# Kernel tuning notes

Measured on AMD Instinct MI355X. Metric: run time of the kernel, lower is better.

Reference implementation:

```python
import jax, jax.numpy as jnp
import numpy as np

C = 256
G = 32  # GroupNorm groups
EPS = 1e-6


def setup_inputs() -> dict:
    key = jax.random.key(0)
    ks = jax.random.split(key, 11)
    B, H, W = 4, 64, 64
    scale = 0.02
    return {
        "x": jax.random.normal(ks[0], (B, C, H, W), dtype=jnp.float32),
        "gn_scale": jnp.ones((C,), jnp.float32),
        "gn_bias": jnp.zeros((C,), jnp.float32),
        "wq": jax.random.normal(ks[1], (C, C), jnp.float32) * scale,
        "bq": jnp.zeros((C,), jnp.float32),
        "wk": jax.random.normal(ks[2], (C, C), jnp.float32) * scale,
        "bk": jnp.zeros((C,), jnp.float32),
        "wv": jax.random.normal(ks[3], (C, C), jnp.float32) * scale,
        "bv": jnp.zeros((C,), jnp.float32),
        "wp": jax.random.normal(ks[4], (C, C), jnp.float32) * scale,
        "bp": jnp.zeros((C,), jnp.float32),
    }


def _group_norm(x, scale, bias):
    b, c, h, w = x.shape
    xr = x.reshape(b, G, c // G, h, w)
    mu = jnp.mean(xr, axis=(2, 3, 4), keepdims=True)
    var = jnp.var(xr, axis=(2, 3, 4), keepdims=True)
    xn = ((xr - mu) * jax.lax.rsqrt(var + EPS)).reshape(b, c, h, w)
    return xn * scale[None, :, None, None] + bias[None, :, None, None]


def _conv1x1(x, w, bch):
    # 1x1 conv == channel-mixing matmul; w is (out_ch, in_ch)
    return jnp.einsum('bchw,dc->bdhw', x, w) + bch[None, :, None, None]


def reference(x, gn_scale, gn_bias, wq, bq, wk, bk, wv, bv, wp, bp):
    b, c, h, w = x.shape
    hn = _group_norm(x, gn_scale, gn_bias)
    q = _conv1x1(hn, wq, bq).reshape(b, c, h * w)  # (b,c,N)
    k = _conv1x1(hn, wk, bk).reshape(b, c, h * w)
    v = _conv1x1(hn, wv, bv).reshape(b, c, h * w)
    # attn[b,i,j] = softmax_j( q_i . k_j / sqrt(c) )
    attn = jax.nn.softmax(jnp.einsum('bci,bcj->bij', q, k) * (c ** -0.5), axis=-1)
    A = jnp.einsum('bcj,bij->bci', v, attn).reshape(b, c, h, w)
    return x + _conv1x1(A, wp, bp)
```

## Files before the change

kernel.cpp:

```cpp
#include <hip/hip_runtime.h>
#include <stdint.h>

#define Bn 4
#define Cn 256
#define Gn 32
#define Nn 4096
#define CGn 8

typedef unsigned short u16;
typedef __attribute__((ext_vector_type(8))) short short8;
typedef __attribute__((ext_vector_type(4))) short short4v;
typedef __attribute__((ext_vector_type(4))) float f32x4;
typedef __attribute__((ext_vector_type(16))) float f32x16;

__device__ __forceinline__ u16 f2bf(float x) {
  uint32_t u = __float_as_uint(x);
  u += 0x7fffu + ((u >> 16) & 1u);
  return (u16)(u >> 16);
}
__device__ __forceinline__ float b2f(u16 v) {
  return __uint_as_float(((uint32_t)v) << 16);
}

__device__ __forceinline__ void gl_lds16(const void* g, void* l) {
  __builtin_amdgcn_global_load_lds(
      (__attribute__((address_space(1))) void*)(uintptr_t)g,
      (__attribute__((address_space(3))) void*)(uintptr_t)l, 16, 0, 0);
}

__device__ __forceinline__ int sw512(int row, int cb) { return row * 512 + ((cb ^ (row & 7)) * 16); }

__global__ void k_cs(const float* __restrict__ wq, const float* __restrict__ wk,
                     const float* __restrict__ wv, const float* __restrict__ wp,
                     const float* __restrict__ bq, const float* __restrict__ bk,
                     const float* __restrict__ bv, const float* __restrict__ x,
                     u16* __restrict__ wqkv, u16* __restrict__ wpb,
                     float* __restrict__ bqkv, float* __restrict__ stats) {
  if (blockIdx.x < 256) {
    const float s = 0.09016844005556021f;
    int i = blockIdx.x * 256 + threadIdx.x;
    wqkv[i]          = f2bf(wq[i] * s);
    wqkv[i + 65536]  = f2bf(wk[i]);
    wqkv[i + 131072] = f2bf(wv[i]);
    wpb[i]           = f2bf(wp[i]);
    if (i < 256) { bqkv[i] = bq[i] * s; bqkv[i + 256] = bk[i]; bqkv[i + 512] = bv[i]; }
  } else {
    int blk = blockIdx.x - 256;
    int grp = blk >> 2, part = blk & 3;
    const float4* base = (const float4*)(x + (size_t)grp * (CGn * Nn) + part * 8192);
    float s = 0.f, s2 = 0.f;
    for (int i = threadIdx.x; i < 2048; i += 256) {
      float4 v = base[i];
      s  += v.x + v.y + v.z + v.w;
      s2 += v.x * v.x + v.y * v.y + v.z * v.z + v.w * v.w;
    }
#pragma unroll
    for (int m = 1; m < 64; m <<= 1) { s += __shfl_xor(s, m, 64); s2 += __shfl_xor(s2, m, 64); }
    __shared__ float ps[4], ps2[4];
    int w = threadIdx.x >> 6;
    if ((threadIdx.x & 63) == 0) { ps[w] = s; ps2[w] = s2; }
    __syncthreads();
    if (threadIdx.x == 0) {
      stats[grp * 8 + part * 2]     = ps[0] + ps[1] + ps[2] + ps[3];
      stats[grp * 8 + part * 2 + 1] = ps2[0] + ps2[1] + ps2[2] + ps2[3];
    }
  }
}

__global__ void k_apply(const float* __restrict__ x, const float* __restrict__ stats,
                        const float* __restrict__ gsc, const float* __restrict__ gbi,
                        u16* __restrict__ hnT) {
  __shared__ __align__(16) char smem[32768];
  __shared__ float smu[Gn], srs[Gn];
  int n0 = blockIdx.x * 64;
  int b = blockIdx.y;
  int tid = threadIdx.x;
  if (tid < Gn) {
    float S = 0.f, S2 = 0.f;
#pragma unroll
    for (int p = 0; p < 4; ++p) {
      S  += stats[(b * Gn + tid) * 8 + p * 2];
      S2 += stats[(b * Gn + tid) * 8 + p * 2 + 1];
    }
    const float inv = 1.f / (CGn * Nn);
    float mu = S * inv;
    float var = S2 * inv - mu * mu;
    smu[tid] = mu;
    srs[tid] = rsqrtf(var + 1e-6f);
  }
  __syncthreads();
  int nl = (tid & 15) * 4;
  int cbase = tid >> 4;
  for (int pass = 0; pass < 16; ++pass) {
    int c = pass * 16 + cbase;
    float4 v = *(const float4*)(x + (size_t)b * Cn * Nn + (size_t)c * Nn + n0 + nl);
    int g = c >> 3;
    float sc = gsc[c] * srs[g];
    float bi = gbi[c] - smu[g] * sc;
    float vals[4] = {v.x, v.y, v.z, v.w};
#pragma unroll
    for (int i = 0; i < 4; ++i) {
      int row = nl + i;
      int off = row * 512 + ((((c >> 3) + row) & 31) * 16) + (c & 7) * 2;
      *(u16*)(smem + off) = f2bf(vals[i] * sc + bi);
    }
  }
  __syncthreads();
#pragma unroll
  for (int p = 0; p < 8; ++p) {
    int idx = p * 256 + tid;
    int row = idx >> 5, pc = idx & 31;
    int gc = (pc - row) & 31;
    short8 v8 = *(const short8*)(smem + row * 512 + pc * 16);
    *(short8*)(hnT + ((size_t)b * Nn + n0 + row) * Cn + gc * 8) = v8;
  }
}

__global__ __launch_bounds__(256, 2)
void k_qkv(const u16* __restrict__ wqkv, const float* __restrict__ bqkv,
           const u16* __restrict__ hnT, u16* __restrict__ qT, u16* __restrict__ kT,
           u16* __restrict__ vv) {
  __shared__ __align__(16) char smem[65536];
  const int tid = threadIdx.x, lane = tid & 63, w = tid >> 6;
  const int quad = (lane >> 4) & 3, low = lane & 15;
  const int d0 = blockIdx.y * 64, b = blockIdx.z;
  const int n_base = blockIdx.x * 256;
  const int which = d0 >> 8;
  const int dl0 = d0 & 255;
  const u16* hb = hnT + (size_t)b * Nn * Cn;
  const int scol = lane & 31;

#define QKV_STAGE(bsel, nt)                                                     \
  {                                                                             \
    _Pragma("unroll") for (int s = 0; s < 8; ++s) {                             \
      int r = w * 16 + s * 2 + (lane >> 5);                                     \
      int gc = (scol - r) & 31;                                                 \
      gl_lds16(hb + (size_t)(n_base + (nt) * 64 + r) * Cn + gc * 8,             \
               smem + (bsel) * 32768 + (w * 16 + s * 2) * 512);                 \
    }                                                                           \
  }

  QKV_STAGE(0, 0);
  short8 af[8];
  {
    const u16* wrow = wqkv + (size_t)(d0 + w * 16 + low) * Cn + quad * 8;
#pragma unroll
    for (int kk = 0; kk < 8; ++kk) af[kk] = *(const short8*)(wrow + kk * 32);
  }
  float bias[4];
#pragma unroll
  for (int r = 0; r < 4; ++r) bias[r] = bqkv[d0 + w * 16 + quad * 4 + r];

  for (int nt = 0; nt < 4; ++nt) {
    if (nt < 3) {
      QKV_STAGE((nt + 1) & 1, nt + 1);
      asm volatile("s_waitcnt vmcnt(10)" ::: "memory");
    } else {
      asm volatile("s_waitcnt vmcnt(0)" ::: "memory");
    }
    asm volatile("s_barrier" ::: "memory");
    char* buf = smem + (nt & 1) * 32768;
    f32x4 acc[4] = {{0.f,0.f,0.f,0.f},{0.f,0.f,0.f,0.f},{0.f,0.f,0.f,0.f},{0.f,0.f,0.f,0.f}};
#pragma unroll
    for (int kk = 0; kk < 8; ++kk)
#pragma unroll
      for (int t = 0; t < 4; ++t) {
        int row = t * 16 + low;
        short8 bf = *(const short8*)(buf + row * 512 + (((kk * 4 + quad) + row) & 31) * 16);
        acc[t] = __builtin_amdgcn_mfma_f32_16x16x32_bf16(af[kk], bf, acc[t], 0, 0, 0);
      }
    asm volatile("s_barrier" ::: "memory");
    char* Q = buf + w * 8192;
    if (which == 2) {
#pragma unroll
      for (int t = 0; t < 4; ++t)
#pragma unroll
        for (int rp = 0; rp < 2; ++rp) {
          uint32_t wv2;
          float f0 = acc[t][2 * rp] + bias[2 * rp];
          float f1 = acc[t][2 * rp + 1] + bias[2 * rp + 1];
          asm("v_cvt_pk_bf16_f32 %0, %1, %2" : "=v"(wv2) : "v"(f0), "v"(f1));
          *(u16*)(Q + (quad * 4 + 2 * rp) * 144 + t * 32 + low * 2) = (u16)wv2;
          *(u16*)(Q + (quad * 4 + 2 * rp + 1) * 144 + t * 32 + low * 2) = (u16)(wv2 >> 16);
        }
#pragma unroll
      for (int s = 0; s < 2; ++s) {
        int slot = s * 64 + lane;
        int row = slot >> 3, ch = slot & 7;
        short8 v8 = *(const short8*)(Q + row * 144 + ch * 16);
        *(short8*)(vv + (size_t)b * Cn * Nn + (size_t)(dl0 + w * 16 + row) * Nn +
                   n_base + nt * 64 + ch * 8) = v8;
      }
    } else {
#pragma unroll
      for (int t = 0; t < 4; ++t) {
        union { uint32_t u[2]; short4v s; } pk;
        float f0 = acc[t][0] + bias[0], f1 = acc[t][1] + bias[1];
        float f2 = acc[t][2] + bias[2], f3 = acc[t][3] + bias[3];
        asm("v_cvt_pk_bf16_f32 %0, %1, %2" : "=v"(pk.u[0]) : "v"(f0), "v"(f1));
        asm("v_cvt_pk_bf16_f32 %0, %1, %2" : "=v"(pk.u[1]) : "v"(f2), "v"(f3));
        *(short4v*)(Q + (t * 16 + low) * 48 + quad * 8) = pk.s;
      }
      u16* dst = (which == 0 ? qT : kT) + (size_t)b * Nn * Cn;
#pragma unroll
      for (int s = 0; s < 2; ++s) {
        int slot = s * 64 + lane;
        int row = slot >> 1, half = slot & 1;
        short8 v8 = *(const short8*)(Q + row * 48 + half * 16);
        *(short8*)(dst + (size_t)(n_base + nt * 64 + row) * Cn + dl0 + w * 16 + half * 8) = v8;
      }
    }
  }
#undef QKV_STAGE
}

__device__ __forceinline__ void flash_stage(char* smem, int bsel, const u16* kTb,
                                            const u16* vb, int j0, int w, int lo,
                                            int kr, int vr, int vp) {
  char* ksb = smem + bsel * 32768;
  char* vsb = ksb + 16384;
#pragma unroll
  for (int s = 0; s < 4; ++s) {
    int j = kr + s * 2;
    int gc = (lo - j) & 31;
    gl_lds16(kTb + (size_t)(j0 + j) * Cn + gc * 8, ksb + (w * 8 + s * 2) * 512);
  }
#pragma unroll
  for (int s = 0; s < 4; ++s) {
    int c = vr + s * 16;
    int gc = (vp - c - (c >> 2)) & 3;
    gl_lds16(vb + (size_t)c * Nn + j0 + gc * 8, vsb + (w * 64 + s * 16) * 64);
  }
}

__global__ __launch_bounds__(256, 2)
void k_flash(const u16* __restrict__ qT, const u16* __restrict__ kT,
             const u16* __restrict__ vv, u16* __restrict__ Op0,
             u16* __restrict__ Op1, u16* __restrict__ Op2, u16* __restrict__ Op3,
             float* __restrict__ lrow) {
  __shared__ __align__(16) char smem[65536];
  const int tid = threadIdx.x, lane = tid & 63, w = tid >> 6;
  const int lo = lane & 31, hi = lane >> 5;
  const int i0 = blockIdx.x * 128;
  const int b = blockIdx.y, jh = blockIdx.z;
  const u16* qTb = qT + (size_t)b * Nn * Cn;
  const u16* kTb = kT + (size_t)b * Nn * Cn;
  const u16* vb  = vv + (size_t)b * Cn * Nn;
  const int u7 = lo + hi;
  const int u9 = lo + hi + (lo >> 2);
  const int kr = w * 8 + hi;
  const int vr = w * 64 + (lane >> 2);
  const int vp = lane & 3;

  flash_stage(smem, 0, kTb, vb, jh * 1024, w, lo, kr, vr, vp);

  short8 qf[16];
  {
    const u16* qrow = qTb + (size_t)(i0 + w * 32 + lo) * Cn + hi * 8;
#pragma unroll
    for (int ks = 0; ks < 16; ++ks) qf[ks] = *(const short8*)(qrow + ks * 16);
  }
  f32x16 Oa[8];
#pragma unroll
  for (int ct = 0; ct < 8; ++ct)
#pragma unroll
    for (int e = 0; e < 16; ++e) Oa[ct][e] = 0.f;
  float l_ = 0.f;

  for (int jt = 0; jt < 32; ++jt) {
    if (jt < 31) {
      flash_stage(smem, (jt + 1) & 1, kTb, vb, jh * 1024 + (jt + 1) * 32, w, lo, kr, vr, vp);
      asm volatile("s_waitcnt vmcnt(8)" ::: "memory");
    } else {
      asm volatile("s_waitcnt vmcnt(0)" ::: "memory");
    }
    asm volatile("s_barrier" ::: "memory");
    const char* ksb = smem + (jt & 1) * 32768;
    const char* vsb = ksb + 16384;

    f32x16 S0;
#pragma unroll
    for (int e = 0; e < 16; ++e) S0[e] = 0.f;
    __builtin_amdgcn_s_setprio(1);
#pragma unroll
    for (int ks = 0; ks < 16; ++ks) {
      int ch = (ks * 2 + u7) & 31;
      short8 a0 = *(const short8*)(ksb + lo * 512 + ch * 16);
      S0 = __builtin_amdgcn_mfma_f32_32x32x16_bf16(a0, qf[ks], S0, 0, 0, 0);
    }
    __builtin_amdgcn_s_setprio(0);
    uint32_t Pp[8];
#pragma unroll
    for (int g = 0; g < 8; ++g) {
      float p0 = __builtin_amdgcn_exp2f(S0[2 * g]);
      float p1 = __builtin_amdgcn_exp2f(S0[2 * g + 1]);
      l_ += p0 + p1;
      asm("v_cvt_pk_bf16_f32 %0, %1, %2" : "=v"(Pp[g]) : "v"(p0), "v"(p1));
    }
#pragma unroll
    for (int kst = 0; kst < 2; ++kst) {
      uint32_t x0 = Pp[4 * kst], x1 = Pp[4 * kst + 1];
      uint32_t y0 = Pp[4 * kst + 2], y1 = Pp[4 * kst + 3];
      asm("v_permlane32_swap_b32 %0, %1" : "+v"(x0), "+v"(y0));
      asm("v_permlane32_swap_b32 %0, %1" : "+v"(x1), "+v"(y1));
      union { uint32_t u[4]; short8 s8; } pu;
      pu.u[0] = x0;
      pu.u[1] = x1;
      pu.u[2] = y0;
      pu.u[3] = y1;
      int ch = (kst * 2 + u9) & 3;
      __builtin_amdgcn_s_setprio(1);
#pragma unroll
      for (int ct = 0; ct < 8; ++ct) {
        short8 vf = *(const short8*)(vsb + (ct * 32 + lo) * 64 + ch * 16);
        Oa[ct] = __builtin_amdgcn_mfma_f32_32x32x16_bf16(vf, pu.s8, Oa[ct], 0, 0, 0);
      }
      __builtin_amdgcn_s_setprio(0);
    }
    asm volatile("s_barrier" ::: "memory");
  }

  l_ += __shfl_xor(l_, 32, 64);
  if (hi == 0)
    lrow[(size_t)jh * (Bn * Nn) + (size_t)b * Nn + i0 + w * 32 + lo] = l_;
  float invl = __builtin_amdgcn_rcpf(l_);
  __syncthreads();
#pragma unroll
  for (int ct = 0; ct < 8; ++ct)
#pragma unroll
    for (int g = 0; g < 4; ++g) {
      union { uint32_t u[2]; short4v s; } pk;
      float f0 = Oa[ct][g * 4 + 0] * invl, f1 = Oa[ct][g * 4 + 1] * invl;
      float f2 = Oa[ct][g * 4 + 2] * invl, f3 = Oa[ct][g * 4 + 3] * invl;
      asm("v_cvt_pk_bf16_f32 %0, %1, %2" : "=v"(pk.u[0]) : "v"(f0), "v"(f1));
      asm("v_cvt_pk_bf16_f32 %0, %1, %2" : "=v"(pk.u[1]) : "v"(f2), "v"(f3));
      int chv = (ct * 4 + g + lo) & 31;
      *(short4v*)(smem + w * 16384 + lo * 512 + chv * 16 + hi * 8) = pk.s;
    }
  __syncthreads();
  u16* Opj = (jh == 0) ? Op0 : (jh == 1) ? Op1 : (jh == 2) ? Op2 : Op3;
  u16* Ob = Opj + ((size_t)b * Nn + i0 + w * 32) * (size_t)Cn;
#pragma unroll
  for (int s = 0; s < 16; ++s) {
    int rr = s * 2 + hi;
    short8 v8 = *(const short8*)(smem + w * 16384 + rr * 512 + lo * 16);
    int gc = (lo - rr) & 31;
    *(short8*)(Ob + (size_t)rr * Cn + gc * 8) = v8;
  }
}

__global__ __launch_bounds__(256, 2)
void k_proj(const u16* __restrict__ wpb, const float* __restrict__ bp,
            const u16* __restrict__ O0, const u16* __restrict__ O1,
            const u16* __restrict__ O2, const u16* __restrict__ O3,
            const float* __restrict__ lrow,
            const float* __restrict__ x, float* __restrict__ out) {
  __shared__ __align__(16) char smem[16384];
  int tid = threadIdx.x, lane = tid & 63, w = tid >> 6, quad = lane >> 4, low = lane & 15;
  int n0 = blockIdx.x * 32, b = blockIdx.z;
#pragma unroll
  for (int p = 0; p < 4; ++p) {
    int slot = p * 256 + tid;
    int row = slot >> 5, pc = slot & 31;
    int gcb = pc ^ (row & 7);
    size_t gbase = ((size_t)b * Nn + n0 + row) * Cn + gcb * 8;
    short8 a0 = *(const short8*)(O0 + gbase);
    short8 a1 = *(const short8*)(O1 + gbase);
    short8 a2 = *(const short8*)(O2 + gbase);
    short8 a3 = *(const short8*)(O3 + gbase);
    int rrow = b * Nn + n0 + row;
    float L = lrow[rrow] + lrow[Bn * Nn + rrow] + lrow[2 * Bn * Nn + rrow] +
              lrow[3 * Bn * Nn + rrow];
    float inv = __builtin_amdgcn_rcpf(L);
    short8 o;
#pragma unroll
    for (int i = 0; i < 8; ++i)
      o[i] = (short)f2bf((b2f((u16)a0[i]) + b2f((u16)a1[i]) + b2f((u16)a2[i]) +
                          b2f((u16)a3[i])) * inv);
    *(short8*)(smem + row * 512 + pc * 16) = o;
  }
  __syncthreads();
  for (int dg = 0; dg < 4; ++dg) {
    short8 af[8];
    {
      const u16* wrow = wpb + (size_t)(dg * 64 + w * 16 + low) * Cn + quad * 8;
#pragma unroll
      for (int kk = 0; kk < 8; ++kk) af[kk] = *(const short8*)(wrow + kk * 32);
    }
    f32x4 acc[2] = {{0.f,0.f,0.f,0.f},{0.f,0.f,0.f,0.f}};
#pragma unroll
    for (int kk = 0; kk < 8; ++kk)
#pragma unroll
      for (int t = 0; t < 2; ++t) {
        short8 bf = *(const short8*)(smem + sw512(t * 16 + low, kk * 4 + quad));
        acc[t] = __builtin_amdgcn_mfma_f32_16x16x32_bf16(af[kk], bf, acc[t], 0, 0, 0);
      }
    int dloc = dg * 64 + w * 16 + quad * 4;
#pragma unroll
    for (int t = 0; t < 2; ++t)
#pragma unroll
      for (int r = 0; r < 4; ++r) {
        size_t idx = (size_t)b * Cn * Nn + (size_t)(dloc + r) * Nn + n0 + t * 16 + low;
        out[idx] = x[idx] + acc[t][r] + bp[dloc + r];
      }
  }
}

extern "C" void kernel_launch(void* const* d_in, const int* in_sizes, int n_in,
                              void* d_out, int out_size, void* d_ws, size_t ws_size,
                              hipStream_t stream) {
  const float* x   = (const float*)d_in[0];
  const float* gsc = (const float*)d_in[1];
  const float* gbi = (const float*)d_in[2];
  const float* wq  = (const float*)d_in[3];
  const float* bq  = (const float*)d_in[4];
  const float* wk  = (const float*)d_in[5];
  const float* bk  = (const float*)d_in[6];
  const float* wv  = (const float*)d_in[7];
  const float* bv  = (const float*)d_in[8];
  const float* wp  = (const float*)d_in[9];
  const float* bp  = (const float*)d_in[10];
  float* out = (float*)d_out;

  char* ws = (char*)d_ws;
  u16*   wqkv  = (u16*)(ws + 0);
  u16*   wpb   = (u16*)(ws + 393216);
  float* bqkv  = (float*)(ws + 524288);
  float* stats = (float*)(ws + 527360);
  float* lrow  = (float*)(ws + 532480);
  u16*   hnT   = (u16*)(ws + 1048576);
  u16*   qT    = (u16*)(ws + 9437184);
  u16*   kT    = (u16*)(ws + 17825792);
  u16*   vv    = (u16*)(ws + 26214400);
  u16*   Op1   = (u16*)(ws + 34603008);
  u16*   Op2   = (u16*)(ws + 42991616);
  u16*   Op3   = (u16*)(ws + 51380224);

  k_cs<<<768, 256, 0, stream>>>(wq, wk, wv, wp, bq, bk, bv, x, wqkv, wpb, bqkv, stats);
  k_apply<<<dim3(64, 4), 256, 0, stream>>>(x, stats, gsc, gbi, hnT);
  k_qkv<<<dim3(16, 12, 4), 256, 0, stream>>>(wqkv, bqkv, hnT, qT, kT, vv);
  k_flash<<<dim3(32, 4, 4), 256, 0, stream>>>(qT, kT, vv, hnT , Op1, Op2, Op3, lrow);
  k_proj<<<dim3(128, 1, 4), 256, 0, stream>>>(wpb, bp, hnT , Op1, Op2, Op3, lrow, x, out);
}
```

Measured before the change: 193.1 us.

## Restructure QKV projection so each block loads a 32-row hn tile once and loops over all output channels

The QKV kernel used to split output channels across the grid, so every block re-staged a 256-row hn tile with double buffering. Now each block stages one 32-row hn tile into LDS once and loops over all 12 groups of 64 output channels, streaming the weights from global or cache. LDS use drops and launch bounds rise to 4 blocks per CU for more occupancy. The cost is that weight fragments are reloaded for every channel group and the weight-load latency is not pipelined. The LDS staging slots are reused between groups without a barrier, but they are private to each wave.

After: 205.7 us. 6.5% more time.

```diff
diff --git a/kernel.cpp b/kernel.cpp
--- a/kernel.cpp
+++ b/kernel.cpp
@@ -116,84 +116,68 @@
   }
 }
 
-__global__ __launch_bounds__(256, 2)
+__global__ __launch_bounds__(256, 4)
 void k_qkv(const u16* __restrict__ wqkv, const float* __restrict__ bqkv,
            const u16* __restrict__ hnT, u16* __restrict__ qT, u16* __restrict__ kT,
            u16* __restrict__ vv) {
-  __shared__ __align__(16) char smem[65536];
+  __shared__ __align__(16) char smem[24576];
   const int tid = threadIdx.x, lane = tid & 63, w = tid >> 6;
   const int quad = (lane >> 4) & 3, low = lane & 15;
-  const int d0 = blockIdx.y * 64, b = blockIdx.z;
-  const int n_base = blockIdx.x * 256;
-  const int which = d0 >> 8;
-  const int dl0 = d0 & 255;
+  const int n0 = blockIdx.x * 32, b = blockIdx.y;
   const u16* hb = hnT + (size_t)b * Nn * Cn;
-  const int scol = lane & 31;
-
-#define QKV_STAGE(bsel, nt)                                                     \
-  {                                                                             \
-    _Pragma("unroll") for (int s = 0; s < 8; ++s) {                             \
-      int r = w * 16 + s * 2 + (lane >> 5);                                     \
-      int gc = (scol - r) & 31;                                                 \
-      gl_lds16(hb + (size_t)(n_base + (nt) * 64 + r) * Cn + gc * 8,             \
-               smem + (bsel) * 32768 + (w * 16 + s * 2) * 512);                 \
-    }                                                                           \
-  }
-
-  QKV_STAGE(0, 0);
-  short8 af[8];
   {
-    const u16* wrow = wqkv + (size_t)(d0 + w * 16 + low) * Cn + quad * 8;
-#pragma unroll
-    for (int kk = 0; kk < 8; ++kk) af[kk] = *(const short8*)(wrow + kk * 32);
-  }
-  float bias[4];
-#pragma unroll
-  for (int r = 0; r < 4; ++r) bias[r] = bqkv[d0 + w * 16 + quad * 4 + r];
-
-  for (int nt = 0; nt < 4; ++nt) {
-    if (nt < 3) {
-      QKV_STAGE((nt + 1) & 1, nt + 1);
-      asm volatile("s_waitcnt vmcnt(10)" ::: "memory");
-    } else {
-      asm volatile("s_waitcnt vmcnt(0)" ::: "memory");
-    }
-    asm volatile("s_barrier" ::: "memory");
-    char* buf = smem + (nt & 1) * 32768;
-    f32x4 acc[4] = {{0.f,0.f,0.f,0.f},{0.f,0.f,0.f,0.f},{0.f,0.f,0.f,0.f},{0.f,0.f,0.f,0.f}};
+    int lo = lane & 31;
+#pragma unroll
+    for (int s = 0; s < 4; ++s) {
+      int r = w * 8 + s * 2 + (lane >> 5);
+      int gc = (lo - r) & 31;
+      gl_lds16(hb + (size_t)(n0 + r) * Cn + gc * 8, smem + (w * 8 + s * 2) * 512);
+    }
+  }
+  asm volatile("s_waitcnt vmcnt(0)" ::: "memory");
+  __syncthreads();
+  char* Q = smem + 16384 + w * 2048;
+  for (int dg = 0; dg < 12; ++dg) {
+    short8 af[8];
+    {
+      const u16* wrow = wqkv + (size_t)(dg * 64 + w * 16 + low) * Cn + quad * 8;
+#pragma unroll
+      for (int kk = 0; kk < 8; ++kk) af[kk] = *(const short8*)(wrow + kk * 32);
+    }
+    float bias[4];
+#pragma unroll
+    for (int r = 0; r < 4; ++r) bias[r] = bqkv[dg * 64 + w * 16 + quad * 4 + r];
+    f32x4 acc[2] = {{0.f,0.f,0.f,0.f},{0.f,0.f,0.f,0.f}};
 #pragma unroll
     for (int kk = 0; kk < 8; ++kk)
 #pragma unroll
-      for (int t = 0; t < 4; ++t) {
+      for (int t = 0; t < 2; ++t) {
         int row = t * 16 + low;
-        short8 bf = *(const short8*)(buf + row * 512 + (((kk * 4 + quad) + row) & 31) * 16);
+        short8 bf = *(const short8*)(smem + row * 512 + (((kk * 4 + quad) + row) & 31) * 16);
         acc[t] = __builtin_amdgcn_mfma_f32_16x16x32_bf16(af[kk], bf, acc[t], 0, 0, 0);
       }
-    asm volatile("s_barrier" ::: "memory");
-    char* Q = buf + w * 8192;
+    int which = dg >> 2, dl0 = (dg & 3) * 64;
     if (which == 2) {
 #pragma unroll
-      for (int t = 0; t < 4; ++t)
+      for (int t = 0; t < 2; ++t)
 #pragma unroll
         for (int rp = 0; rp < 2; ++rp) {
           uint32_t wv2;
           float f0 = acc[t][2 * rp] + bias[2 * rp];
           float f1 = acc[t][2 * rp + 1] + bias[2 * rp + 1];
           asm("v_cvt_pk_bf16_f32 %0, %1, %2" : "=v"(wv2) : "v"(f0), "v"(f1));
-          *(u16*)(Q + (quad * 4 + 2 * rp) * 144 + t * 32 + low * 2) = (u16)wv2;
-          *(u16*)(Q + (quad * 4 + 2 * rp + 1) * 144 + t * 32 + low * 2) = (u16)(wv2 >> 16);
+          *(u16*)(Q + (quad * 4 + 2 * rp) * 72 + t * 32 + low * 2) = (u16)wv2;
+          *(u16*)(Q + (quad * 4 + 2 * rp + 1) * 72 + t * 32 + low * 2) = (u16)(wv2 >> 16);
         }
-#pragma unroll
-      for (int s = 0; s < 2; ++s) {
-        int slot = s * 64 + lane;
-        int row = slot >> 3, ch = slot & 7;
-        short8 v8 = *(const short8*)(Q + row * 144 + ch * 16);
+      {
+        int row = lane >> 2, ch = lane & 3;
+        short8 v8 = *(const short8*)(Q + row * 72 + ch * 16);
         *(short8*)(vv + (size_t)b * Cn * Nn + (size_t)(dl0 + w * 16 + row) * Nn +
-                   n_base + nt * 64 + ch * 8) = v8;
+                   n0 + ch * 8) = v8;
       }
     } else {
 #pragma unroll
-      for (int t = 0; t < 4; ++t) {
+      for (int t = 0; t < 2; ++t) {
         union { uint32_t u[2]; short4v s; } pk;
         float f0 = acc[t][0] + bias[0], f1 = acc[t][1] + bias[1];
         float f2 = acc[t][2] + bias[2], f3 = acc[t][3] + bias[3];
@@ -202,16 +186,13 @@
         *(short4v*)(Q + (t * 16 + low) * 48 + quad * 8) = pk.s;
       }
       u16* dst = (which == 0 ? qT : kT) + (size_t)b * Nn * Cn;
-#pragma unroll
-      for (int s = 0; s < 2; ++s) {
-        int slot = s * 64 + lane;
-        int row = slot >> 1, half = slot & 1;
+      {
+        int row = lane >> 1, half = lane & 1;
         short8 v8 = *(const short8*)(Q + row * 48 + half * 16);
-        *(short8*)(dst + (size_t)(n_base + nt * 64 + row) * Cn + dl0 + w * 16 + half * 8) = v8;
-      }
-    }
-  }
-#undef QKV_STAGE
+        *(short8*)(dst + (size_t)(n0 + row) * Cn + dl0 + w * 16 + half * 8) = v8;
+      }
+    }
+  }
 }
 
 __device__ __forceinline__ void flash_stage(char* smem, int bsel, const u16* kTb,
@@ -438,7 +419,7 @@
 
   k_cs<<<768, 256, 0, stream>>>(wq, wk, wv, wp, bq, bk, bv, x, wqkv, wpb, bqkv, stats);
   k_apply<<<dim3(64, 4), 256, 0, stream>>>(x, stats, gsc, gbi, hnT);
-  k_qkv<<<dim3(16, 12, 4), 256, 0, stream>>>(wqkv, bqkv, hnT, qT, kT, vv);
+  k_qkv<<<dim3(128, 4), 256, 0, stream>>>(wqkv, bqkv, hnT, qT, kT, vv);
   k_flash<<<dim3(32, 4, 4), 256, 0, stream>>>(qT, kT, vv, hnT , Op1, Op2, Op3, lrow);
   k_proj<<<dim3(128, 1, 4), 256, 0, stream>>>(wpb, bp, hnT , Op1, Op2, Op3, lrow, x, out);
 }
```
